# Optimization experiments

Hardware: AMD Instinct MI355X
Metric: run time of the kernel (lower is better)

Reference implementation:

```python
import jax, jax.numpy as jnp
import numpy as np

B, T, I, H, N = 32, 512, 128, 128, 16  # batch, time, input, hidden_per_rnn, num_rnn


def setup_inputs() -> dict:
    key = jax.random.key(0)
    k1, k2, k3 = jax.random.split(key, 3)
    x = jax.random.normal(k1, (B, T, I), dtype=jnp.float32)
    # scale weights like torch RNN default init (uniform ~ 1/sqrt(Htot)) to keep relu recurrence stable
    s = 1.0 / np.sqrt(H * N)
    W_ih = jax.random.normal(k2, (H * N, I), dtype=jnp.float32) * s
    W_hh = jax.random.normal(k3, (H * N, H * N), dtype=jnp.float32) * s
    b_ih = jnp.zeros((H * N,), dtype=jnp.float32)
    b_hh = jnp.zeros((H * N,), dtype=jnp.float32)
    return {"x": x, "W_ih": W_ih, "W_hh": W_hh, "b_ih": b_ih, "b_hh": b_hh, "num_rnn": N}


def reference(x, W_ih, W_hh, b_ih, b_hh, num_rnn):
    Bq, Tq, _ = x.shape
    Htot = W_hh.shape[0]
    n = int(num_rnn)
    h = Htot // n
    # block-diagonal mask: keep only the n diagonal (h x h) blocks of W_hh
    idx = jnp.arange(n)
    blocks = W_hh.reshape(n, h, n, h)[idx, :, idx, :]  # (n, h, h)
    # input projection + biases done once outside the recurrence
    pre = jnp.einsum('bti,hi->bth', x, W_ih) + b_ih + b_hh  # (B, T, Htot)
    pre = pre.reshape(Bq, Tq, n, h).transpose(1, 0, 2, 3)  # (T, B, n, h)

    def step(hprev, p):
        # h_t = relu(pre_t + h_{t-1} @ W_block^T) per independent block
        hnew = jax.nn.relu(p + jnp.einsum('bnh,ngh->bng', hprev, blocks))
        return hnew, hnew

    h0 = jnp.zeros((Bq, n, h), dtype=x.dtype)
    _, hs = jax.lax.scan(step, h0, pre)  # (T, B, n, h)
    hs_all = hs.transpose(1, 0, 2, 3)  # (B, T, num_rnn, hidden_size)
    hidden = hs_all[:, -1].reshape(Bq, n * h)[None]  # (1, B, Htot), detached in torch
    hidden = jax.lax.stop_gradient(hidden)
    return hs_all, hidden
```

## Files before the change

### kernel.cpp

```cpp
#include <hip/hip_runtime.h>
#include <hip/hip_bf16.h>

#define BB   32
#define TT   512
#define II   128
#define HH   128
#define NR   16
#define HTOT 2048

typedef __attribute__((ext_vector_type(8))) short short8;
typedef __attribute__((ext_vector_type(4))) float f32x4;

static __device__ __forceinline__ short f2bf(float f) {
    union { __hip_bfloat16 h; short s; } u;
    u.h = __float2bfloat16(f);
    return u.s;
}
static __device__ __forceinline__ float bf2f(unsigned short u) {
    return __uint_as_float(((unsigned int)u) << 16);
}

__global__ __launch_bounds__(512, 2) void msml_pre2(
    const float* __restrict__ x,
    const float* __restrict__ Wih,
    const float* __restrict__ bih,
    const float* __restrict__ bhh,
    unsigned short* __restrict__ pre)
{
    const int mx = blockIdx.x;
    const int tid = threadIdx.x;
    const int w = tid >> 6, l = tid & 63;
    const int q = l >> 4;
    const int r0 = mx * 64;
    const int b  = r0 >> 9;
    const int t0 = r0 & 511;
    const int g  = b >> 4, m = b & 15;

    __shared__ short A[64 * 136];

    {
        const int row = tid >> 3, cb = tid & 7;
        const float4* xs = reinterpret_cast<const float4*>(
            x + (size_t)(r0 + row) * II + cb * 16);
        short* dst = &A[row * 136 + cb * 16];
#pragma unroll
        for (int i = 0; i < 4; ++i) {
            float4 v = xs[i];
            *reinterpret_cast<short4*>(dst + 4 * i) =
                make_short4(f2bf(v.x), f2bf(v.y), f2bf(v.z), f2bf(v.w));
        }
    }
    __syncthreads();

    const int j = w * 16 + (l & 15);

    for (int n = 0; n < NR; ++n) {
        short8 bw[4];
        {
            const float* wb = Wih + (size_t)(n * HH + j) * II + q * 8;
#pragma unroll
            for (int kt = 0; kt < 4; ++kt) {
                float4 u0 = *reinterpret_cast<const float4*>(wb + kt * 32);
                float4 u1 = *reinterpret_cast<const float4*>(wb + kt * 32 + 4);
                short8 s;
                s[0] = f2bf(u0.x); s[1] = f2bf(u0.y); s[2] = f2bf(u0.z); s[3] = f2bf(u0.w);
                s[4] = f2bf(u1.x); s[5] = f2bf(u1.y); s[6] = f2bf(u1.z); s[7] = f2bf(u1.w);
                bw[kt] = s;
            }
        }
        const float bias = bih[n * HH + j] + bhh[n * HH + j];
        const size_t ng = (size_t)(n * 2 + g);

#pragma unroll
        for (int mt = 0; mt < 4; ++mt) {
            const short* ap = &A[(mt * 16 + (l & 15)) * 136 + q * 8];
            f32x4 acc = {0.f, 0.f, 0.f, 0.f};
#pragma unroll
            for (int kt = 0; kt < 4; ++kt) {
                short8 a = *reinterpret_cast<const short8*>(ap + kt * 32);
                acc = __builtin_amdgcn_mfma_f32_16x16x32_bf16(a, bw[kt], acc, 0, 0, 0);
            }
#pragma unroll
            for (int r = 0; r < 4; ++r) {
                const int t = t0 + mt * 16 + q * 4 + r;
                pre[((ng * TT + t) * 16 + m) * 128 + j] = (unsigned short)f2bf(acc[r] + bias);
            }
        }
    }
}

__global__ __launch_bounds__(512, 2) void msml_recur(
    const float* __restrict__ Whh,
    const unsigned short* __restrict__ pre,
    float* __restrict__ out)
{
    const int n = blockIdx.x;
    const int g = blockIdx.y;
    const int tid = threadIdx.x;
    const int w = tid >> 6, l = tid & 63;
    const int q = l >> 4;
    const int j = w * 16 + (l & 15);

    __shared__ short Hl[2][16 * 136];

    short8 bw[4];
#pragma unroll
    for (int kt = 0; kt < 4; ++kt) {
        const float* wb = Whh + (size_t)(n * HH + j) * HTOT + n * HH + kt * 32 + q * 8;
        float4 u0 = *reinterpret_cast<const float4*>(wb);
        float4 u1 = *reinterpret_cast<const float4*>(wb + 4);
        short8 s;
        s[0] = f2bf(u0.x); s[1] = f2bf(u0.y); s[2] = f2bf(u0.z); s[3] = f2bf(u0.w);
        s[4] = f2bf(u1.x); s[5] = f2bf(u1.y); s[6] = f2bf(u1.z); s[7] = f2bf(u1.w);
        bw[kt] = s;
    }

    for (int i = tid; i < 16 * 136; i += 512) Hl[0][i] = 0;

    const unsigned short* pb = pre + ((size_t)(n * 2 + g) * TT) * 2048 + (q * 4) * 128 + j;
    unsigned short pA0, pA1, pA2, pA3, pB0, pB1, pB2, pB3;
    { const unsigned short* pp = pb;        pA0 = pp[0]; pA1 = pp[128]; pA2 = pp[256]; pA3 = pp[384]; }
    { const unsigned short* pp = pb + 2048; pB0 = pp[0]; pB1 = pp[128]; pB2 = pp[256]; pB3 = pp[384]; }

    const size_t MS = (size_t)TT * HTOT;
    float* ob = out + (size_t)(g * 16 + q * 4) * MS + n * HH + j;

    __syncthreads();

#define RSTEP(HRD, HWR, P0, P1, P2, P3, TCUR)                                      \
    {                                                                              \
        const short* hp = &HRD[(l & 15) * 136 + q * 8];                            \
        f32x4 acc = {0.f, 0.f, 0.f, 0.f};                                          \
        _Pragma("unroll")                                                          \
        for (int kt = 0; kt < 4; ++kt) {                                           \
            short8 a = *reinterpret_cast<const short8*>(hp + kt * 32);             \
            acc = __builtin_amdgcn_mfma_f32_16x16x32_bf16(a, bw[kt], acc, 0, 0, 0);\
        }                                                                          \
        float h0 = fmaxf(acc[0] + bf2f(P0), 0.f);                                  \
        float h1 = fmaxf(acc[1] + bf2f(P1), 0.f);                                  \
        float h2 = fmaxf(acc[2] + bf2f(P2), 0.f);                                  \
        float h3 = fmaxf(acc[3] + bf2f(P3), 0.f);                                  \
        { int tn = (TCUR) + 2 < TT ? (TCUR) + 2 : TT - 1;                          \
          const unsigned short* pp = pb + (size_t)tn * 2048;                       \
          P0 = pp[0]; P1 = pp[128]; P2 = pp[256]; P3 = pp[384]; }                  \
        float* oo = ob + (size_t)(TCUR) * HTOT;                                    \
        oo[0] = h0; oo[MS] = h1; oo[2 * MS] = h2; oo[3 * MS] = h3;                 \
        HWR[(q * 4 + 0) * 136 + j] = f2bf(h0);                                     \
        HWR[(q * 4 + 1) * 136 + j] = f2bf(h1);                                     \
        HWR[(q * 4 + 2) * 136 + j] = f2bf(h2);                                     \
        HWR[(q * 4 + 3) * 136 + j] = f2bf(h3);                                     \
        if ((TCUR) == TT - 1) {                                                    \
            float* hh = out + (size_t)BB * TT * HTOT                               \
                        + (size_t)(g * 16 + q * 4) * HTOT + n * HH + j;            \
            hh[0] = h0; hh[HTOT] = h1; hh[2 * HTOT] = h2; hh[3 * HTOT] = h3;       \
        }                                                                          \
        __builtin_amdgcn_sched_barrier(0);                                         \
        asm volatile("s_waitcnt lgkmcnt(0)");                                      \
        __builtin_amdgcn_s_barrier();                                              \
        __builtin_amdgcn_sched_barrier(0);                                         \
    }

    short* hb0 = &Hl[0][0];
    short* hb1 = &Hl[1][0];
    for (int t = 0; t < TT; t += 2) {
        RSTEP(hb0, hb1, pA0, pA1, pA2, pA3, t)
        RSTEP(hb1, hb0, pB0, pB1, pB2, pB3, t + 1)
    }
#undef RSTEP
}

__global__ __launch_bounds__(512, 4) void msml_fused2(
    const float* __restrict__ x,
    const float* __restrict__ Wih,
    const float* __restrict__ Whh,
    const float* __restrict__ bih,
    const float* __restrict__ bhh,
    float* __restrict__ out)
{
    const int n    = blockIdx.x;
    const int b    = blockIdx.y;
    const int tid  = threadIdx.x;
    const int wave = tid >> 6;
    const int lane = tid & 63;
    const int s    = lane >> 4;
    const int j    = wave * 16 + (lane & 15);
    const int row  = n * HH + j;

    float wih[32], whh[32];
    {
        const float4* wi4 = reinterpret_cast<const float4*>(Wih + (size_t)row * II);
        const float4* wh4 = reinterpret_cast<const float4*>(Whh + (size_t)row * HTOT + n * HH);
#pragma unroll
        for (int k = 0; k < 8; ++k) {
            float4 a = wi4[4 * k + s];
            wih[4*k+0] = a.x; wih[4*k+1] = a.y; wih[4*k+2] = a.z; wih[4*k+3] = a.w;
            float4 c = wh4[4 * k + s];
            whh[4*k+0] = c.x; whh[4*k+1] = c.y; whh[4*k+2] = c.z; whh[4*k+3] = c.w;
        }
    }
    const float bias0 = (s == 0) ? (bih[row] + bhh[row]) : 0.0f;

    __shared__ float hs[2][HH];
    if (tid < HH) hs[0][tid] = 0.0f;

    const float* xrow = x + (size_t)b * TT * II;
    float* orow = out + (size_t)b * TT * HTOT + (size_t)n * HH + j;

    float accx;
    {
        const float4* xv = reinterpret_cast<const float4*>(xrow);
        float a0 = bias0, a1 = 0.f, a2 = 0.f, a3 = 0.f;
#pragma unroll
        for (int k = 0; k < 8; ++k) {
            float4 v = xv[4 * k + s];
            a0 += wih[4*k+0] * v.x; a1 += wih[4*k+1] * v.y;
            a2 += wih[4*k+2] * v.z; a3 += wih[4*k+3] * v.w;
        }
        accx = (a0 + a1) + (a2 + a3);
    }
    __syncthreads();

    float hn = 0.0f;
    int buf = 0;
    for (int t = 0; t < TT; ++t) {
        float4 xn[8];
        if (t + 1 < TT) {
            const float4* xv = reinterpret_cast<const float4*>(xrow + (size_t)(t + 1) * II);
#pragma unroll
            for (int k = 0; k < 8; ++k) xn[k] = xv[4 * k + s];
        }
        const float4* hv = reinterpret_cast<const float4*>(hs[buf]);
        float a0 = accx, a1 = 0.f, a2 = 0.f, a3 = 0.f;
#pragma unroll
        for (int k = 0; k < 8; ++k) {
            float4 v = hv[4 * k + s];
            a0 += whh[4*k+0] * v.x; a1 += whh[4*k+1] * v.y;
            a2 += whh[4*k+2] * v.z; a3 += whh[4*k+3] * v.w;
        }
        float sum = (a0 + a1) + (a2 + a3);
        sum += __shfl_xor(sum, 16);
        sum += __shfl_xor(sum, 32);
        hn = fmaxf(sum, 0.0f);

        if (s == 0) {
            orow[(size_t)t * HTOT] = hn;
            hs[buf ^ 1][j] = hn;
        }
        {
            float b0 = bias0, b1 = 0.f, b2 = 0.f, b3 = 0.f;
#pragma unroll
            for (int k = 0; k < 8; ++k) {
                b0 += wih[4*k+0] * xn[k].x; b1 += wih[4*k+1] * xn[k].y;
                b2 += wih[4*k+2] * xn[k].z; b3 += wih[4*k+3] * xn[k].w;
            }
            accx = (b0 + b1) + (b2 + b3);
        }
        buf ^= 1;
        __syncthreads();
    }

    if (s == 0)
        out[(size_t)BB * TT * HTOT + (size_t)b * HTOT + row] = hn;
}

extern "C" void kernel_launch(void* const* d_in, const int* in_sizes, int n_in,
                              void* d_out, int out_size, void* d_ws, size_t ws_size,
                              hipStream_t stream) {
    const float* x   = (const float*)d_in[0];
    const float* Wih = (const float*)d_in[1];
    const float* Whh = (const float*)d_in[2];
    const float* bih = (const float*)d_in[3];
    const float* bhh = (const float*)d_in[4];
    float* out = (float*)d_out;

    const size_t pre_bytes = (size_t)NR * 2 * TT * 16 * 128 * sizeof(unsigned short);

    if (ws_size >= pre_bytes && d_ws != nullptr) {
        unsigned short* pre = (unsigned short*)d_ws;
        msml_pre2<<<dim3(256), 512, 0, stream>>>(x, Wih, bih, bhh, pre);
        msml_recur<<<dim3(NR, 2), 512, 0, stream>>>(Whh, pre, out);
    } else {
        msml_fused2<<<dim3(NR, BB), 512, 0, stream>>>(x, Wih, Whh, bih, bhh, out);
    }
}
```

Before: 210.2 us.

## Split recurrence across more blocks with 8 batch rows each, widen pre-GEMM grid

The recurrence kernel now runs 64 blocks instead of 32. Each block handles 8 batch rows per RNN block, and only half the lanes (q<2) write results, so the sequential 512-step chain is spread over more CUs. The input-projection kernel is split across 4 y-blocks, each covering 4 of the 16 RNNs, which raises parallelism and occupancy. In exchange, half of each MFMA's rows go unused and the recurrent weights are loaded redundantly by twice as many blocks.

```diff
diff --git a/kernel.cpp b/kernel.cpp
--- a/kernel.cpp
+++ b/kernel.cpp
@@ -20,7 +20,7 @@
     return __uint_as_float(((unsigned int)u) << 16);
 }
 
-__global__ __launch_bounds__(512, 2) void msml_pre2(
+__global__ __launch_bounds__(512, 4) void msml_pre4(
     const float* __restrict__ x,
     const float* __restrict__ Wih,
     const float* __restrict__ bih,
@@ -28,6 +28,7 @@
     unsigned short* __restrict__ pre)
 {
     const int mx = blockIdx.x;
+    const int ny = blockIdx.y;
     const int tid = threadIdx.x;
     const int w = tid >> 6, l = tid & 63;
     const int q = l >> 4;
@@ -54,7 +55,8 @@
 
     const int j = w * 16 + (l & 15);
 
-    for (int n = 0; n < NR; ++n) {
+    for (int nn = 0; nn < 4; ++nn) {
+        const int n = ny * 4 + nn;
         short8 bw[4];
         {
             const float* wb = Wih + (size_t)(n * HH + j) * II + q * 8;
@@ -89,19 +91,24 @@
     }
 }
 
-__global__ __launch_bounds__(512, 2) void msml_recur(
+__global__ __launch_bounds__(512, 2) void msml_recur8b(
     const float* __restrict__ Whh,
     const unsigned short* __restrict__ pre,
     float* __restrict__ out)
 {
-    const int n = blockIdx.x;
-    const int g = blockIdx.y;
+    const int n  = blockIdx.x;
+    const int gg = blockIdx.y;
     const int tid = threadIdx.x;
     const int w = tid >> 6, l = tid & 63;
     const int q = l >> 4;
-    const int j = w * 16 + (l & 15);
-
-    __shared__ short Hl[2][16 * 136];
+    const int c = l & 15;
+    const int j = w * 16 + c;
+    const int g  = gg >> 1;
+    const int m0 = (gg & 1) * 8;
+    const bool act = (q < 2);
+    const int qb = q & 1;
+
+    __shared__ short Hl[2][8 * 136];
 
     short8 bw[4];
 #pragma unroll
@@ -115,21 +122,22 @@
         bw[kt] = s;
     }
 
-    for (int i = tid; i < 16 * 136; i += 512) Hl[0][i] = 0;
-
-    const unsigned short* pb = pre + ((size_t)(n * 2 + g) * TT) * 2048 + (q * 4) * 128 + j;
+    for (int i = tid; i < 8 * 136; i += 512) Hl[0][i] = 0;
+
+    const unsigned short* pb = pre + ((size_t)(n * 2 + g) * TT) * 2048
+                               + (m0 + qb * 4) * 128 + j;
     unsigned short pA0, pA1, pA2, pA3, pB0, pB1, pB2, pB3;
     { const unsigned short* pp = pb;        pA0 = pp[0]; pA1 = pp[128]; pA2 = pp[256]; pA3 = pp[384]; }
     { const unsigned short* pp = pb + 2048; pB0 = pp[0]; pB1 = pp[128]; pB2 = pp[256]; pB3 = pp[384]; }
 
     const size_t MS = (size_t)TT * HTOT;
-    float* ob = out + (size_t)(g * 16 + q * 4) * MS + n * HH + j;
+    float* ob = out + (size_t)(g * 16 + m0 + qb * 4) * MS + n * HH + j;
 
     __syncthreads();
 
 #define RSTEP(HRD, HWR, P0, P1, P2, P3, TCUR)                                      \
     {                                                                              \
-        const short* hp = &HRD[(l & 15) * 136 + q * 8];                            \
+        const short* hp = &HRD[(c & 7) * 136 + q * 8];                             \
         f32x4 acc = {0.f, 0.f, 0.f, 0.f};                                          \
         _Pragma("unroll")                                                          \
         for (int kt = 0; kt < 4; ++kt) {                                           \
@@ -143,16 +151,18 @@
         { int tn = (TCUR) + 2 < TT ? (TCUR) + 2 : TT - 1;                          \
           const unsigned short* pp = pb + (size_t)tn * 2048;                       \
           P0 = pp[0]; P1 = pp[128]; P2 = pp[256]; P3 = pp[384]; }                  \
-        float* oo = ob + (size_t)(TCUR) * HTOT;                                    \
-        oo[0] = h0; oo[MS] = h1; oo[2 * MS] = h2; oo[3 * MS] = h3;                 \
-        HWR[(q * 4 + 0) * 136 + j] = f2bf(h0);                                     \
-        HWR[(q * 4 + 1) * 136 + j] = f2bf(h1);                                     \
-        HWR[(q * 4 + 2) * 136 + j] = f2bf(h2);                                     \
-        HWR[(q * 4 + 3) * 136 + j] = f2bf(h3);                                     \
-        if ((TCUR) == TT - 1) {                                                    \
-            float* hh = out + (size_t)BB * TT * HTOT                               \
-                        + (size_t)(g * 16 + q * 4) * HTOT + n * HH + j;            \
-            hh[0] = h0; hh[HTOT] = h1; hh[2 * HTOT] = h2; hh[3 * HTOT] = h3;       \
+        if (act) {                                                                 \
+            float* oo = ob + (size_t)(TCUR) * HTOT;                                \
+            oo[0] = h0; oo[MS] = h1; oo[2 * MS] = h2; oo[3 * MS] = h3;             \
+            HWR[(q * 4 + 0) * 136 + j] = f2bf(h0);                                 \
+            HWR[(q * 4 + 1) * 136 + j] = f2bf(h1);                                 \
+            HWR[(q * 4 + 2) * 136 + j] = f2bf(h2);                                 \
+            HWR[(q * 4 + 3) * 136 + j] = f2bf(h3);                                 \
+            if ((TCUR) == TT - 1) {                                                \
+                float* hh = out + (size_t)BB * TT * HTOT                           \
+                            + (size_t)(g * 16 + m0 + q * 4) * HTOT + n * HH + j;   \
+                hh[0] = h0; hh[HTOT] = h1; hh[2 * HTOT] = h2; hh[3 * HTOT] = h3;   \
+            }                                                                      \
         }                                                                          \
         __builtin_amdgcn_sched_barrier(0);                                         \
         asm volatile("s_waitcnt lgkmcnt(0)");                                      \
@@ -277,8 +287,8 @@
 
     if (ws_size >= pre_bytes && d_ws != nullptr) {
         unsigned short* pre = (unsigned short*)d_ws;
-        msml_pre2<<<dim3(256), 512, 0, stream>>>(x, Wih, bih, bhh, pre);
-        msml_recur<<<dim3(NR, 2), 512, 0, stream>>>(Whh, pre, out);
+        msml_pre4<<<dim3(256, 4), 512, 0, stream>>>(x, Wih, bih, bhh, pre);
+        msml_recur8b<<<dim3(NR, 4), 512, 0, stream>>>(Whh, pre, out);
     } else {
         msml_fused2<<<dim3(NR, BB), 512, 0, stream>>>(x, Wih, Whh, bih, bhh, out);
     }
```

Measured after the change: 225.3 us. 1.07x slower.
